# Kernel tuning notes

Measured on AMD Instinct MI355X. Metric: run time of the kernel, lower is better.

Reference implementation:

```python
import jax, jax.numpy as jnp
import numpy as np

EXCHANGE_RATIO = 0.5


def setup_inputs() -> dict:
    key = jax.random.key(0)
    k1, k2, k3, k4 = jax.random.split(key, 4)
    B, C, L = 8, 512, 4096
    x1 = jax.random.normal(k1, (B, C, L), dtype=jnp.float32)
    x2 = jax.random.normal(k2, (B, C, L), dtype=jnp.float32)
    bn1 = jax.random.normal(k3, (C,), dtype=jnp.float32)
    bn2 = jax.random.normal(k4, (C,), dtype=jnp.float32)
    return {"x1": x1, "x2": x2, "bn1": bn1, "bn2": bn2}


def _nontop_indices(bn, topk):
    # channels NOT in topk of |bn|, in ascending index order (matches torch
    # boolean-mask indexing semantics)
    a = jnp.abs(bn)
    C = bn.shape[0]
    _, idx = jax.lax.top_k(a, topk)
    mask = jnp.zeros((C,), dtype=bool).at[idx].set(True)
    # stable argsort of bool puts False (non-top) first, in ascending index order
    nontop = jnp.argsort(mask, stable=True)[: C - topk]
    return nontop


def reference(x1, x2, bn1, bn2):
    C = bn1.shape[0]
    topk = int(C * (1.0 - EXCHANGE_RATIO))  # static: 256
    nontop1 = _nontop_indices(bn1, topk)
    nontop2 = _nontop_indices(bn2, topk)
    # y1 keeps x1's top channels, takes x2's non-top channels (order-aligned)
    y1 = x1.at[:, nontop1, :].set(x2[:, nontop2, :])
    # y2 keeps x2's top channels, takes x1's non-top channels
    y2 = x2.at[:, nontop2, :].set(x1[:, nontop1, :])
    return (y1, y2)
```

## Files before the change

kernel.cpp:

```cpp
#include <hip/hip_runtime.h>
#include <math.h>

#define C_CH   512
#define TOPK   256
#define B_N    8
#define L_LEN  4096
#define L4     (L_LEN / 4)
#define ROWS_T (B_N * C_CH)
#define NJOBS  (2 * ROWS_T)
#define NBLK   2048

typedef float nf4 __attribute__((ext_vector_type(4)));

__global__ __launch_bounds__(C_CH) void build_maps(
        const float* __restrict__ bn1,
        const float* __restrict__ bn2,
        int* __restrict__ map1,
        int* __restrict__ map2) {
    __shared__ float2 a12[C_CH];
    __shared__ int nt1[C_CH - TOPK], nt2[C_CH - TOPK];
    __shared__ int wsum1[8], wsum2[8];
    const int t = threadIdx.x;
    const float v1 = fabsf(bn1[t]);
    const float v2 = fabsf(bn2[t]);
    a12[t] = make_float2(v1, v2);
    __syncthreads();

    int r1 = 0, r2 = 0;
#pragma unroll 8
    for (int j = 0; j < C_CH; ++j) {
        const float2 bj = a12[j];
        r1 += (bj.x > v1) || (bj.x == v1 && j < t);
        r2 += (bj.y > v2) || (bj.y == v2 && j < t);
    }
    const bool non1 = (r1 >= TOPK);
    const bool non2 = (r2 >= TOPK);

    const unsigned long long m1 = __ballot(non1);
    const unsigned long long m2 = __ballot(non2);
    const int lane = t & 63, w = t >> 6;
    const unsigned long long below = (1ULL << lane) - 1ULL;
    const int lp1 = __popcll(m1 & below);
    const int lp2 = __popcll(m2 & below);
    if (lane == 0) { wsum1[w] = __popcll(m1); wsum2[w] = __popcll(m2); }
    __syncthreads();
    int base1 = 0, base2 = 0;
#pragma unroll
    for (int i = 0; i < 8; ++i) {
        base1 += (i < w) ? wsum1[i] : 0;
        base2 += (i < w) ? wsum2[i] : 0;
    }
    const int p1 = base1 + lp1;
    const int p2 = base2 + lp2;
    if (non1) nt1[p1] = t;
    if (non2) nt2[p2] = t;
    __syncthreads();

    map1[t] = non1 ? (C_CH + nt2[p1]) : t;
    map2[t] = non2 ? (C_CH + nt1[p2]) : t;
}

struct Job { const float4* __restrict__ src; float4* __restrict__ dst; };

__device__ __forceinline__ Job job_addr(int job,
        const float4* __restrict__ x1, const float4* __restrict__ x2,
        const int* __restrict__ map1, const int* __restrict__ map2,
        float4* __restrict__ y1, float4* __restrict__ y2) {
    const int rr = job & (ROWS_T - 1);
    const int c = rr & (C_CH - 1);
    const int b = rr >> 9;
    const bool second = job >= ROWS_T;
    const int m = second ? map2[c] : map1[c];
    const float4* base = second ? ((m < C_CH) ? x2 : x1)
                                : ((m < C_CH) ? x1 : x2);
    Job j;
    j.src = base + ((size_t)((b << 9) | (m & (C_CH - 1))) << 10);
    j.dst = (second ? y2 : y1) + ((size_t)rr << 10);
    return j;
}

__global__ __launch_bounds__(256) void exchange_copy(
        const float4* __restrict__ x1,
        const float4* __restrict__ x2,
        const int* __restrict__ map1,
        const int* __restrict__ map2,
        float4* __restrict__ y1,
        float4* __restrict__ y2) {
    const int t = threadIdx.x;
    const int blk = blockIdx.x;

    const Job j0 = job_addr(blk,            x1, x2, map1, map2, y1, y2);
    const Job j1 = job_addr(blk + NBLK,     x1, x2, map1, map2, y1, y2);
    const Job j2 = job_addr(blk + 2 * NBLK, x1, x2, map1, map2, y1, y2);
    const Job j3 = job_addr(blk + 3 * NBLK, x1, x2, map1, map2, y1, y2);

    float4 r0[4], r1[4], r2[4], r3[4];

#pragma unroll
    for (int k = 0; k < 4; ++k) r0[k] = j0.src[t + 256 * k];
#pragma unroll
    for (int k = 0; k < 4; ++k) r1[k] = j1.src[t + 256 * k];
#pragma unroll
    for (int k = 0; k < 4; ++k)
        __builtin_nontemporal_store(*(const nf4*)&r0[k], (nf4*)j0.dst + t + 256 * k);
#pragma unroll
    for (int k = 0; k < 4; ++k) r2[k] = j2.src[t + 256 * k];
#pragma unroll
    for (int k = 0; k < 4; ++k)
        __builtin_nontemporal_store(*(const nf4*)&r1[k], (nf4*)j1.dst + t + 256 * k);
#pragma unroll
    for (int k = 0; k < 4; ++k) r3[k] = j3.src[t + 256 * k];
#pragma unroll
    for (int k = 0; k < 4; ++k)
        __builtin_nontemporal_store(*(const nf4*)&r2[k], (nf4*)j2.dst + t + 256 * k);
#pragma unroll
    for (int k = 0; k < 4; ++k)
        __builtin_nontemporal_store(*(const nf4*)&r3[k], (nf4*)j3.dst + t + 256 * k);
}

extern "C" void kernel_launch(void* const* d_in, const int* in_sizes, int n_in,
                              void* d_out, int out_size, void* d_ws, size_t ws_size,
                              hipStream_t stream) {
    const float* x1  = (const float*)d_in[0];
    const float* x2  = (const float*)d_in[1];
    const float* bn1 = (const float*)d_in[2];
    const float* bn2 = (const float*)d_in[3];

    float* y1 = (float*)d_out;
    float* y2 = (float*)d_out + (B_N * C_CH * L_LEN);

    int* map1 = (int*)d_ws;
    int* map2 = map1 + C_CH;

    build_maps<<<1, C_CH, 0, stream>>>(bn1, bn2, map1, map2);

    exchange_copy<<<NBLK, 256, 0, stream>>>(
        (const float4*)x1, (const float4*)x2, map1, map2,
        (float4*)y1, (float4*)y2);
}
```

Before: 266.3 us.

## Switch exchange copy to scatter by source row with XCD-aware block order

The copy kernel now reads source rows sequentially and scatters each one to its mapped destination row, instead of gathering from mapped source rows. Block IDs are remapped so consecutive jobs are spread across the eight XCDs. Nontemporal stores are replaced with plain stores. The aim is more regular, streaming reads and better spread of memory traffic across chiplets, at the cost of possibly worse write-side caching behaviour for a pure streaming copy.

```diff
diff --git a/kernel.cpp b/kernel.cpp
--- a/kernel.cpp
+++ b/kernel.cpp
@@ -9,8 +9,6 @@
 #define ROWS_T (B_N * C_CH)
 #define NJOBS  (2 * ROWS_T)
 #define NBLK   2048
-
-typedef float nf4 __attribute__((ext_vector_type(4)));
 
 __global__ __launch_bounds__(C_CH) void build_maps(
         const float* __restrict__ bn1,
@@ -62,21 +60,21 @@
 
 struct Job { const float4* __restrict__ src; float4* __restrict__ dst; };
 
-__device__ __forceinline__ Job job_addr(int job,
+__device__ __forceinline__ Job job_addr(int j,
         const float4* __restrict__ x1, const float4* __restrict__ x2,
         const int* __restrict__ map1, const int* __restrict__ map2,
         float4* __restrict__ y1, float4* __restrict__ y2) {
-    const int rr = job & (ROWS_T - 1);
+    const int rr = j & (ROWS_T - 1);
     const int c = rr & (C_CH - 1);
     const int b = rr >> 9;
-    const bool second = job >= ROWS_T;
-    const int m = second ? map2[c] : map1[c];
-    const float4* base = second ? ((m < C_CH) ? x2 : x1)
-                                : ((m < C_CH) ? x1 : x2);
-    Job j;
-    j.src = base + ((size_t)((b << 9) | (m & (C_CH - 1))) << 10);
-    j.dst = (second ? y2 : y1) + ((size_t)rr << 10);
-    return j;
+    const bool isX2 = j >= ROWS_T;
+    const int m = isX2 ? map2[c] : map1[c];
+    const bool other = (m >= C_CH);
+    Job jb;
+    jb.src = (isX2 ? x2 : x1) + ((size_t)rr << 10);
+    float4* yb = isX2 ? (other ? y1 : y2) : (other ? y2 : y1);
+    jb.dst = yb + ((size_t)((b << 9) | (m & (C_CH - 1))) << 10);
+    return jb;
 }
 
 __global__ __launch_bounds__(256) void exchange_copy(
@@ -87,7 +85,8 @@
         float4* __restrict__ y1,
         float4* __restrict__ y2) {
     const int t = threadIdx.x;
-    const int blk = blockIdx.x;
+    const int bid = blockIdx.x;
+    const int blk = (bid & 7) * (NBLK / 8) + (bid >> 3);
 
     const Job j0 = job_addr(blk,            x1, x2, map1, map2, y1, y2);
     const Job j1 = job_addr(blk + NBLK,     x1, x2, map1, map2, y1, y2);
@@ -101,21 +100,17 @@
 #pragma unroll
     for (int k = 0; k < 4; ++k) r1[k] = j1.src[t + 256 * k];
 #pragma unroll
-    for (int k = 0; k < 4; ++k)
-        __builtin_nontemporal_store(*(const nf4*)&r0[k], (nf4*)j0.dst + t + 256 * k);
+    for (int k = 0; k < 4; ++k) j0.dst[t + 256 * k] = r0[k];
 #pragma unroll
     for (int k = 0; k < 4; ++k) r2[k] = j2.src[t + 256 * k];
 #pragma unroll
-    for (int k = 0; k < 4; ++k)
-        __builtin_nontemporal_store(*(const nf4*)&r1[k], (nf4*)j1.dst + t + 256 * k);
+    for (int k = 0; k < 4; ++k) j1.dst[t + 256 * k] = r1[k];
 #pragma unroll
     for (int k = 0; k < 4; ++k) r3[k] = j3.src[t + 256 * k];
 #pragma unroll
-    for (int k = 0; k < 4; ++k)
-        __builtin_nontemporal_store(*(const nf4*)&r2[k], (nf4*)j2.dst + t + 256 * k);
+    for (int k = 0; k < 4; ++k) j2.dst[t + 256 * k] = r2[k];
 #pragma unroll
-    for (int k = 0; k < 4; ++k)
-        __builtin_nontemporal_store(*(const nf4*)&r3[k], (nf4*)j3.dst + t + 256 * k);
+    for (int k = 0; k < 4; ++k) j3.dst[t + 256 * k] = r3[k];
 }
 
 extern "C" void kernel_launch(void* const* d_in, const int* in_sizes, int n_in,
```

After: 272.6 us. +2.4%, slower.
